# Kernel optimization log

Hardware: AMD Instinct MI355X
Metric: run time of the kernel (lower is better)

The kernel has to match this reference:

```python
import jax, jax.numpy as jnp
import numpy as np

N = 100000   # nodes
E = 1000000  # edges (avg degree 10)
F_IN, H1, H2, C = 128, 64, 64, 16


def setup_inputs() -> dict:
    key = jax.random.key(0)
    ks = jax.random.split(key, 10)
    x = jax.random.normal(ks[0], (N, F_IN), dtype=jnp.float32)
    edge_src = jax.random.randint(ks[1], (E,), 0, N, dtype=jnp.int32)
    edge_dst = jax.random.randint(ks[2], (E,), 0, N, dtype=jnp.int32)
    # normalized-adjacency-like positive edge weights (~1/deg scale)
    edge_val = jax.random.uniform(ks[3], (E,), dtype=jnp.float32) * 0.1
    def glorot(k, fan_in, fan_out):
        s = np.float32(1.0 / np.sqrt(fan_in))
        return jax.random.normal(k, (fan_in, fan_out), dtype=jnp.float32) * s
    W1 = glorot(ks[4], F_IN, H1)
    W2 = glorot(ks[5], H1, H2)
    W3 = glorot(ks[6], H2, C)
    b1 = jnp.zeros((H1,), jnp.float32)
    b2 = jnp.zeros((H2,), jnp.float32)
    b3 = jnp.zeros((C,), jnp.float32)
    return {"x": x, "edge_val": edge_val, "W1": W1, "b1": b1,
            "W2": W2, "b2": b2, "W3": W3, "b3": b3,
            "edge_src": edge_src, "edge_dst": edge_dst}


def gcn_layer(h, W, b, edge_src, edge_dst, edge_val):
    # support = h @ W ; out = spmm(adj, support) + b
    support = h @ W                                  # [N, d_out]
    msg = support[edge_src] * edge_val[:, None]      # [E, d_out] gather + scale
    agg = jax.ops.segment_sum(msg, edge_dst, num_segments=N)  # scatter-add
    return agg + b


def reference(x, edge_val, W1, b1, W2, b2, W3, b3, edge_src, edge_dst):
    # eval mode: F.dropout(training=False) is identity
    h = jax.nn.relu(gcn_layer(x, W1, b1, edge_src, edge_dst, edge_val))
    h = jax.nn.relu(gcn_layer(h, W2, b2, edge_src, edge_dst, edge_val))
    return gcn_layer(h, W3, b3, edge_src, edge_dst, edge_val)  # [N, C] logits
```

## Files before the change

kernel.cpp:

```cpp
#include <hip/hip_runtime.h>
#include <stdint.h>

#define N_NODES 100000
#define N_EDGES 1000000
#define NBUCK 98

typedef __attribute__((ext_vector_type(8))) __bf16 bf16x8;
typedef __attribute__((ext_vector_type(4))) float f32x4;

static __device__ __forceinline__ float bf2f(unsigned short u) {
    return __uint_as_float(((unsigned int)u) << 16);
}
static __device__ __forceinline__ unsigned short f2bf(float f) {
    unsigned int u = __float_as_uint(f);
    unsigned int r = (u + 0x7FFFu + ((u >> 16) & 1u)) >> 16;
    return (unsigned short)r;
}
static __device__ __forceinline__ float4 ld4_half(const unsigned short* p) {
    ushort4 u = *(const ushort4*)p;
    return make_float4(bf2f(u.x), bf2f(u.y), bf2f(u.z), bf2f(u.w));
}
static __device__ __forceinline__ void st4_half(unsigned short* p, float4 f) {
    ushort4 u;
    u.x = f2bf(f.x); u.y = f2bf(f.y); u.z = f2bf(f.z); u.w = f2bf(f.w);
    *(ushort4*)p = u;
}
static __device__ __forceinline__ void st8_half(unsigned short* p, const float* f) {
    int4 u;
    u.x = (int)(((unsigned)f2bf(f[0])) | (((unsigned)f2bf(f[1])) << 16));
    u.y = (int)(((unsigned)f2bf(f[2])) | (((unsigned)f2bf(f[3])) << 16));
    u.z = (int)(((unsigned)f2bf(f[4])) | (((unsigned)f2bf(f[5])) << 16));
    u.w = (int)(((unsigned)f2bf(f[6])) | (((unsigned)f2bf(f[7])) << 16));
    *(int4*)p = u;
}

static __device__ __forceinline__ float ldf(const void* p, size_t i, int bf) {
    return bf ? bf2f(((const unsigned short*)p)[i]) : ((const float*)p)[i];
}
static __device__ __forceinline__ float4 ldf4(const void* p, size_t i, int bf) {
    if (bf) return ld4_half((const unsigned short*)p + i);
    return *(const float4*)((const float*)p + i);
}

__global__ __launch_bounds__(256) void detect_kernel(const unsigned short* __restrict__ xs,
                                                     int* __restrict__ flag) {
    __shared__ int sz;
    if (threadIdx.x == 0) sz = 0;
    __syncthreads();
    int z = 0;
    for (int i = threadIdx.x; i < 1024; i += 256) {
        float av = fabsf(bf2f(xs[2 * i]));
        if (!(av <= 1048576.0f) || (av != 0.0f && av < 9.5367431640625e-07f)) z++;
    }
    atomicAdd(&sz, z);
    __syncthreads();
    if (threadIdx.x == 0) *flag = (sz > 256) ? 0 : 1;
}

__global__ __launch_bounds__(256) void bhist_kernel(const int* __restrict__ dst,
                                                    int* __restrict__ bcount) {
    __shared__ int cnt[NBUCK];
    int tid = threadIdx.x;
    for (int i = tid; i < NBUCK; i += 256) cnt[i] = 0;
    __syncthreads();
    int e0 = blockIdx.x * 4096;
#pragma unroll
    for (int i = 0; i < 16; ++i) {
        int e = e0 + i * 256 + tid;
        if (e < N_EDGES) atomicAdd(&cnt[dst[e] >> 10], 1);
    }
    __syncthreads();
    for (int i = tid; i < NBUCK; i += 256) {
        int c = cnt[i];
        if (c) atomicAdd(&bcount[i], c);
    }
}

__global__ __launch_bounds__(128) void bscan_kernel(const int* __restrict__ bcount,
                                                    int* __restrict__ bstart,
                                                    int* __restrict__ bcursor) {
    __shared__ int sh[128];
    int tid = threadIdx.x;
    int v = (tid < NBUCK) ? bcount[tid] : 0;
    sh[tid] = v;
    __syncthreads();
    for (int off = 1; off < 128; off <<= 1) {
        int t = 0;
        if (tid >= off) t = sh[tid - off];
        __syncthreads();
        if (tid >= off) sh[tid] += t;
        __syncthreads();
    }
    if (tid < NBUCK) {
        int excl = sh[tid] - v;
        bstart[tid] = excl;
        bcursor[tid] = excl;
    }
    if (tid == NBUCK - 1) bstart[NBUCK] = sh[tid];
}

__global__ __launch_bounds__(256) void part_kernel(const int* __restrict__ src,
                                                   const int* __restrict__ dst,
                                                   const void* __restrict__ val,
                                                   int* __restrict__ bcursor,
                                                   int2* __restrict__ part,
                                                   const int* __restrict__ flagp) {
    __shared__ int cnt[NBUCK];
    __shared__ int base[NBUCK];
    const int bf = *flagp;
    const int tid = threadIdx.x;
    const int e0 = blockIdx.x * 2048;
    for (int i = tid; i < NBUCK; i += 256) cnt[i] = 0;
    __syncthreads();
    int rank[8], bkt[8], pk[8], vb[8];
#pragma unroll
    for (int i = 0; i < 8; ++i) {
        int e = e0 + i * 256 + tid;
        bkt[i] = -1;
        if (e < N_EDGES) {
            int d = dst[e];
            int b = d >> 10;
            bkt[i] = b;
            pk[i] = src[e] | ((d & 1023) << 17);
            vb[i] = __float_as_int(ldf(val, e, bf));
            rank[i] = atomicAdd(&cnt[b], 1);
        }
    }
    __syncthreads();
    for (int i = tid; i < NBUCK; i += 256) {
        int c = cnt[i];
        base[i] = c ? atomicAdd(&bcursor[i], c) : 0;
    }
    __syncthreads();
#pragma unroll
    for (int i = 0; i < 8; ++i) {
        if (bkt[i] >= 0) part[(size_t)base[bkt[i]] + rank[i]] = make_int2(pk[i], vb[i]);
    }
}

__global__ __launch_bounds__(512) void place_kernel(const int* __restrict__ bstart,
                                                    const int2* __restrict__ part,
                                                    int* __restrict__ row_start,
                                                    int2* __restrict__ csr_rec) {
    __shared__ int cnt[1024];
    __shared__ int sums[512];
    const int tid = threadIdx.x;
    const int b = blockIdx.x;
    const int row0 = b << 10;
    const int nrows = min(1024, N_NODES - row0);
    const int s = bstart[b], e = bstart[b + 1];

    for (int i = tid; i < 1024; i += 512) cnt[i] = 0;
    __syncthreads();
    for (int j = s + tid; j < e; j += 512) {
        unsigned p = (unsigned)part[j].x;
        atomicAdd(&cnt[p >> 17], 1);
    }
    __syncthreads();
    int a0 = cnt[2 * tid], a1 = cnt[2 * tid + 1];
    int ts = a0 + a1;
    sums[tid] = ts;
    __syncthreads();
    for (int off = 1; off < 512; off <<= 1) {
        int t = 0;
        if (tid >= off) t = sums[tid - off];
        __syncthreads();
        if (tid >= off) sums[tid] += t;
        __syncthreads();
    }
    int excl = sums[tid] - ts;
    cnt[2 * tid] = s + excl;
    cnt[2 * tid + 1] = s + excl + a0;
    if (2 * tid < nrows)     row_start[row0 + 2 * tid] = s + excl;
    if (2 * tid + 1 < nrows) row_start[row0 + 2 * tid + 1] = s + excl + a0;
    if (b == NBUCK - 1 && tid == 0) row_start[N_NODES] = e;
    __syncthreads();
    for (int j = s + tid; j < e; j += 512) {
        int2 r = part[j];
        unsigned p = (unsigned)r.x;
        int pos = atomicAdd(&cnt[p >> 17], 1);
        csr_rec[pos] = make_int2((int)(p & 0x1FFFFu), r.y);
    }
}


static __device__ __forceinline__ void duo_gather64(const unsigned short* __restrict__ supc,
                                                    const int2* __restrict__ csr_rec,
                                                    int s, int b1, int e,
                                                    float a0[8], float a1[8]) {
    if (s >= e) return;
    int2 r[8];
#pragma unroll
    for (int t = 0; t < 8; ++t) r[t] = csr_rec[min(s + t, e - 1)];
    for (int j = s; j < e; j += 8) {
        int4 sp[8];
#pragma unroll
        for (int t = 0; t < 8; ++t) sp[t] = *(const int4*)(supc + (size_t)r[t].x * 64);
        float wv[8];
#pragma unroll
        for (int t = 0; t < 8; ++t) wv[t] = (j + t < e) ? __int_as_float(r[t].y) : 0.0f;
        int jn = j + 8;
        if (jn < e) {
#pragma unroll
            for (int t = 0; t < 8; ++t) r[t] = csr_rec[min(jn + t, e - 1)];
        }
#pragma unroll
        for (int t = 0; t < 8; ++t) {
            float w0 = (j + t < b1) ? wv[t] : 0.0f;
            float w1 = wv[t] - w0;
            int q[4] = {sp[t].x, sp[t].y, sp[t].z, sp[t].w};
#pragma unroll
            for (int c = 0; c < 4; ++c) {
                float flo = __uint_as_float(((unsigned)q[c]) << 16);
                float fhi = __uint_as_float(((unsigned)q[c]) & 0xffff0000u);
                a0[2 * c]     += w0 * flo; a0[2 * c + 1] += w0 * fhi;
                a1[2 * c]     += w1 * flo; a1[2 * c + 1] += w1 * fhi;
            }
        }
    }
}

static __device__ __forceinline__ void quad_gather16(const unsigned short* __restrict__ supc,
                                                     const int2* __restrict__ csr_rec,
                                                     int s, int b1, int b2, int b3, int e,
                                                     float a[4][8]) {
    if (s >= e) return;
    int2 r[8];
#pragma unroll
    for (int t = 0; t < 8; ++t) r[t] = csr_rec[min(s + t, e - 1)];
    for (int j = s; j < e; j += 8) {
        int4 sp[8];
#pragma unroll
        for (int t = 0; t < 8; ++t) sp[t] = *(const int4*)(supc + (size_t)r[t].x * 16);
        float wv[8];
#pragma unroll
        for (int t = 0; t < 8; ++t) wv[t] = (j + t < e) ? __int_as_float(r[t].y) : 0.0f;
        int jn = j + 8;
        if (jn < e) {
#pragma unroll
            for (int t = 0; t < 8; ++t) r[t] = csr_rec[min(jn + t, e - 1)];
        }
#pragma unroll
        for (int t = 0; t < 8; ++t) {
            int idx = j + t;
            float c0 = (idx < b1) ? wv[t] : 0.0f;
            float c1 = (idx < b2) ? wv[t] : 0.0f;
            float c2 = (idx < b3) ? wv[t] : 0.0f;
            float w0 = c0, w1 = c1 - c0, w2 = c2 - c1, w3 = wv[t] - c2;
            int q[4] = {sp[t].x, sp[t].y, sp[t].z, sp[t].w};
#pragma unroll
            for (int c = 0; c < 4; ++c) {
                float flo = __uint_as_float(((unsigned)q[c]) << 16);
                float fhi = __uint_as_float(((unsigned)q[c]) & 0xffff0000u);
                a[0][2 * c] += w0 * flo; a[0][2 * c + 1] += w0 * fhi;
                a[1][2 * c] += w1 * flo; a[1][2 * c + 1] += w1 * fhi;
                a[2][2 * c] += w2 * flo; a[2][2 * c + 1] += w2 * fhi;
                a[3][2 * c] += w3 * flo; a[3][2 * c + 1] += w3 * fhi;
            }
        }
    }
}

template <int K, int M, bool DYNIN>
__global__ __launch_bounds__(256, 4) void mgemm_kernel(const void* __restrict__ hv_,
                                                       const void* __restrict__ W,
                                                       unsigned short* __restrict__ out,
                                                       const int* __restrict__ flagp) {
    constexpr int KP = K + 8;
    constexpr int NC = M / 16;
    constexpr int NK = K / 32;
    constexpr int NT = (N_NODES + 63) / 64;

    __shared__ unsigned short wt[M][KP];

    const int bf = *flagp;
    const int tid = threadIdx.x;

    for (int i = tid; i < K * M; i += 256) {
        int k = i / M, m = i % M;
        wt[m][k] = f2bf(ldf(W, i, bf));
    }
    __syncthreads();

    const int lane = tid & 63;
    const int qd = lane >> 4;
    const int ln = lane & 15;
    const int wrow = (tid >> 6) * 16;

    for (int tile = blockIdx.x; tile < NT; tile += gridDim.x) {
        const int row = tile * 64 + wrow + ln;
        const bool ok = row < N_NODES;

        f32x4 acc[NC];
#pragma unroll
        for (int c = 0; c < NC; ++c) acc[c] = (f32x4){0.f, 0.f, 0.f, 0.f};

#pragma unroll
        for (int ks = 0; ks < NK; ++ks) {
            bf16x8 a;
            if (ok) {
                const size_t base = (size_t)row * K + ks * 32 + qd * 8;
                if (DYNIN && !bf) {
                    const float* xp = (const float*)hv_ + base;
                    float4 f0 = *(const float4*)xp;
                    float4 f1 = *(const float4*)(xp + 4);
                    ushort4 uu[2];
                    uu[0].x = f2bf(f0.x); uu[0].y = f2bf(f0.y); uu[0].z = f2bf(f0.z); uu[0].w = f2bf(f0.w);
                    uu[1].x = f2bf(f1.x); uu[1].y = f2bf(f1.y); uu[1].z = f2bf(f1.z); uu[1].w = f2bf(f1.w);
                    a = *(const bf16x8*)uu;
                } else {
                    a = *(const bf16x8*)((const unsigned short*)hv_ + base);
                }
            } else {
                a = (bf16x8)(__bf16)0.0f;
            }
#pragma unroll
            for (int c = 0; c < NC; ++c) {
                bf16x8 b = *(const bf16x8*)&wt[c * 16 + ln][ks * 32 + qd * 8];
                acc[c] = __builtin_amdgcn_mfma_f32_16x16x32_bf16(a, b, acc[c], 0, 0, 0);
            }
        }

#pragma unroll
        for (int c = 0; c < NC; ++c) {
#pragma unroll
            for (int r = 0; r < 4; ++r) {
                int orow = tile * 64 + wrow + qd * 4 + r;
                if (orow < N_NODES) out[(size_t)orow * M + c * 16 + ln] = f2bf(acc[c][r]);
            }
        }
    }
}

template <int MOUT>
__global__ __launch_bounds__(256) void fused_kernel(const unsigned short* __restrict__ support,
                                                    const int* __restrict__ row_start,
                                                    const int2* __restrict__ csr_rec,
                                                    const void* __restrict__ bias,
                                                    const void* __restrict__ W,
                                                    unsigned short* __restrict__ out,
                                                    const int* __restrict__ flagp) {
    constexpr int K = 64, KP = 72;
    constexpr int NC = MOUT / 16;
    constexpr int NK = 2;
    constexpr int NT = (N_NODES + 63) / 64;

    __shared__ unsigned short agg[64][KP];
    __shared__ unsigned short wt[MOUT][KP];

    const int bf = *flagp;
    const int tid = threadIdx.x;

    for (int i = tid; i < K * MOUT; i += 256) {
        int k = i / MOUT, m = i % MOUT;
        wt[m][k] = f2bf(ldf(W, i, bf));
    }
    __syncthreads();

    const int lane = tid & 63;
    const int qd = lane >> 4;
    const int ln = lane & 15;
    const int wrow = (tid >> 6) * 16;

    const int grp = tid >> 3;
    const int cc = tid & 7;
    float bias8[8];
#pragma unroll
    for (int c = 0; c < 8; ++c) bias8[c] = ldf(bias, cc * 8 + c, bf);
    const unsigned short* supc = support + cc * 8;

    for (int tile = blockIdx.x; tile < NT; tile += gridDim.x) {
        const int r0 = tile * 64 + grp * 2;
        int s  = row_start[min(r0 + 0, N_NODES)];
        int b1 = row_start[min(r0 + 1, N_NODES)];
        int e  = row_start[min(r0 + 2, N_NODES)];

        float a0[8], a1[8];
#pragma unroll
        for (int c = 0; c < 8; ++c) { a0[c] = bias8[c]; a1[c] = bias8[c]; }
        duo_gather64(supc, csr_rec, s, b1, e, a0, a1);
#pragma unroll
        for (int c = 0; c < 8; ++c) {
            a0[c] = fmaxf(a0[c], 0.f);
            a1[c] = fmaxf(a1[c], 0.f);
        }
        st8_half(&agg[grp * 2 + 0][cc * 8], a0);
        st8_half(&agg[grp * 2 + 1][cc * 8], a1);
        __syncthreads();

        f32x4 macc[NC];
#pragma unroll
        for (int c = 0; c < NC; ++c) macc[c] = (f32x4){0.f, 0.f, 0.f, 0.f};
#pragma unroll
        for (int ks = 0; ks < NK; ++ks) {
            bf16x8 a = *(const bf16x8*)&agg[wrow + ln][ks * 32 + qd * 8];
#pragma unroll
            for (int c = 0; c < NC; ++c) {
                bf16x8 b = *(const bf16x8*)&wt[c * 16 + ln][ks * 32 + qd * 8];
                macc[c] = __builtin_amdgcn_mfma_f32_16x16x32_bf16(a, b, macc[c], 0, 0, 0);
            }
        }

#pragma unroll
        for (int c = 0; c < NC; ++c) {
#pragma unroll
            for (int r = 0; r < 4; ++r) {
                int orow = tile * 64 + wrow + qd * 4 + r;
                if (orow < N_NODES) out[(size_t)orow * MOUT + c * 16 + ln] = f2bf(macc[c][r]);
            }
        }
        __syncthreads();
    }
}

template <bool DYNOUT>
__global__ __launch_bounds__(256) void spmm16_kernel(const unsigned short* __restrict__ support,
                                                     const int* __restrict__ row_start,
                                                     const int2* __restrict__ csr_rec,
                                                     const void* __restrict__ bias,
                                                     void* __restrict__ out_,
                                                     const int* __restrict__ flagp) {
    constexpr int M = 16;
    int bf = *flagp;
    int tid = threadIdx.x;
    int grp = tid >> 1;
    int cc = tid & 1;
    int r0 = blockIdx.x * 512 + grp * 4;
    if (r0 >= N_NODES) return;
    int s  = row_start[min(r0 + 0, N_NODES)];
    int b1 = row_start[min(r0 + 1, N_NODES)];
    int b2 = row_start[min(r0 + 2, N_NODES)];
    int b3 = row_start[min(r0 + 3, N_NODES)];
    int e  = row_start[min(r0 + 4, N_NODES)];
    float a[4][8];
#pragma unroll
    for (int k = 0; k < 4; ++k)
#pragma unroll
        for (int c = 0; c < 8; ++c) a[k][c] = ldf(bias, cc * 8 + c, bf);
    quad_gather16(support + cc * 8, csr_rec, s, b1, b2, b3, e, a);
#pragma unroll
    for (int k = 0; k < 4; ++k) {
        int row = r0 + k;
        if (row < N_NODES) {
            if (DYNOUT && !bf) {
                float* op = (float*)out_ + (size_t)row * M + cc * 8;
                *(float4*)op = make_float4(a[k][0], a[k][1], a[k][2], a[k][3]);
                *(float4*)(op + 4) = make_float4(a[k][4], a[k][5], a[k][6], a[k][7]);
            } else {
                st8_half((unsigned short*)out_ + (size_t)row * M + cc * 8, a[k]);
            }
        }
    }
}

extern "C" void kernel_launch(void* const* d_in, const int* in_sizes, int n_in,
                              void* d_out, int out_size, void* d_ws, size_t ws_size,
                              hipStream_t stream) {
    (void)in_sizes; (void)n_in; (void)out_size; (void)ws_size;
    const void* x  = d_in[0];
    const void* ev = d_in[1];
    const void* W1 = d_in[2];
    const void* b1 = d_in[3];
    const void* W2 = d_in[4];
    const void* b2 = d_in[5];
    const void* W3 = d_in[6];
    const void* b3 = d_in[7];
    const int* esrc = (const int*)d_in[8];
    const int* edst = (const int*)d_in[9];

    char* ws = (char*)d_ws;
    size_t off = 0;
    auto alloc = [&](size_t bytes) -> void* {
        void* p = ws + off;
        off = (off + bytes + 255) & ~(size_t)255;
        return p;
    };
    unsigned short* A = (unsigned short*)alloc((size_t)N_NODES * 64 * 2);
    unsigned short* B = (unsigned short*)alloc((size_t)N_NODES * 64 * 2);
    int* row_start  = (int*)alloc((size_t)(N_NODES + 1) * 4);
    int* bcount     = (int*)alloc(512);
    int* bstart     = (int*)alloc(512);
    int* bcursor    = (int*)alloc(512);
    int2* csr_rec   = (int2*)alloc((size_t)N_EDGES * 8);
    int* flagp      = (int*)alloc(256);
    int2* part      = (int2*)A;

    detect_kernel<<<1, 256, 0, stream>>>((const unsigned short*)x, flagp);

    hipMemsetAsync(bcount, 0, 512, stream);
    bhist_kernel<<<(N_EDGES + 4095) / 4096, 256, 0, stream>>>(edst, bcount);
    bscan_kernel<<<1, 128, 0, stream>>>(bcount, bstart, bcursor);
    part_kernel<<<(N_EDGES + 2047) / 2048, 256, 0, stream>>>(esrc, edst, ev, bcursor, part, flagp);
    place_kernel<<<NBUCK, 512, 0, stream>>>(bstart, part, row_start, csr_rec);

    const int NT = (N_NODES + 63) / 64;

    mgemm_kernel<128, 64, true><<<1024, 256, 0, stream>>>(x, W1, A, flagp);
    fused_kernel<64><<<NT, 256, 0, stream>>>(A, row_start, csr_rec, b1, W2, B, flagp);
    fused_kernel<16><<<NT, 256, 0, stream>>>(B, row_start, csr_rec, b2, W3, A, flagp);
    spmm16_kernel<true><<<(N_NODES + 511) / 512, 256, 0, stream>>>(A, row_start, csr_rec, b3, d_out, flagp);
}
```

Baseline: 260.5 us.

## Drop bucket histogram pass with fixed-capacity buckets; one tile per block

```diff
diff --git a/kernel.cpp b/kernel.cpp
--- a/kernel.cpp
+++ b/kernel.cpp
@@ -4,6 +4,7 @@
 #define N_NODES 100000
 #define N_EDGES 1000000
 #define NBUCK 98
+#define CAP 12288
 
 typedef __attribute__((ext_vector_type(8))) __bf16 bf16x8;
 typedef __attribute__((ext_vector_type(4))) float f32x4;
@@ -43,7 +44,8 @@
 }
 
 __global__ __launch_bounds__(256) void detect_kernel(const unsigned short* __restrict__ xs,
-                                                     int* __restrict__ flag) {
+                                                     int* __restrict__ flag,
+                                                     int* __restrict__ bcursor) {
     __shared__ int sz;
     if (threadIdx.x == 0) sz = 0;
     __syncthreads();
@@ -53,50 +55,9 @@
         if (!(av <= 1048576.0f) || (av != 0.0f && av < 9.5367431640625e-07f)) z++;
     }
     atomicAdd(&sz, z);
+    if (threadIdx.x < NBUCK) bcursor[threadIdx.x] = threadIdx.x * CAP;
     __syncthreads();
     if (threadIdx.x == 0) *flag = (sz > 256) ? 0 : 1;
-}
-
-__global__ __launch_bounds__(256) void bhist_kernel(const int* __restrict__ dst,
-                                                    int* __restrict__ bcount) {
-    __shared__ int cnt[NBUCK];
-    int tid = threadIdx.x;
-    for (int i = tid; i < NBUCK; i += 256) cnt[i] = 0;
-    __syncthreads();
-    int e0 = blockIdx.x * 4096;
-#pragma unroll
-    for (int i = 0; i < 16; ++i) {
-        int e = e0 + i * 256 + tid;
-        if (e < N_EDGES) atomicAdd(&cnt[dst[e] >> 10], 1);
-    }
-    __syncthreads();
-    for (int i = tid; i < NBUCK; i += 256) {
-        int c = cnt[i];
-        if (c) atomicAdd(&bcount[i], c);
-    }
-}
-
-__global__ __launch_bounds__(128) void bscan_kernel(const int* __restrict__ bcount,
-                                                    int* __restrict__ bstart,
-                                                    int* __restrict__ bcursor) {
-    __shared__ int sh[128];
-    int tid = threadIdx.x;
-    int v = (tid < NBUCK) ? bcount[tid] : 0;
-    sh[tid] = v;
-    __syncthreads();
-    for (int off = 1; off < 128; off <<= 1) {
-        int t = 0;
-        if (tid >= off) t = sh[tid - off];
-        __syncthreads();
-        if (tid >= off) sh[tid] += t;
-        __syncthreads();
-    }
-    if (tid < NBUCK) {
-        int excl = sh[tid] - v;
-        bstart[tid] = excl;
-        bcursor[tid] = excl;
-    }
-    if (tid == NBUCK - 1) bstart[NBUCK] = sh[tid];
 }
 
 __global__ __launch_bounds__(256) void part_kernel(const int* __restrict__ src,
@@ -138,22 +99,42 @@
     }
 }
 
-__global__ __launch_bounds__(512) void place_kernel(const int* __restrict__ bstart,
+__global__ __launch_bounds__(512) void place_kernel(const int* __restrict__ bcursor,
                                                     const int2* __restrict__ part,
                                                     int* __restrict__ row_start,
                                                     int2* __restrict__ csr_rec) {
     __shared__ int cnt[1024];
     __shared__ int sums[512];
+    __shared__ int sh_s, sh_cnt, sh_total;
     const int tid = threadIdx.x;
     const int b = blockIdx.x;
     const int row0 = b << 10;
     const int nrows = min(1024, N_NODES - row0);
-    const int s = bstart[b], e = bstart[b + 1];
+
+    if (tid < 128) sums[tid] = (tid < NBUCK) ? (bcursor[tid] - tid * CAP) : 0;
+    __syncthreads();
+    for (int off = 1; off < 128; off <<= 1) {
+        int t = 0;
+        if (tid < 128 && tid >= off) t = sums[tid - off];
+        __syncthreads();
+        if (tid < 128 && tid >= off) sums[tid] += t;
+        __syncthreads();
+    }
+    if (tid == 0) {
+        sh_s = (b > 0) ? sums[b - 1] : 0;
+        sh_cnt = bcursor[b] - b * CAP;
+        sh_total = sums[NBUCK - 1];
+    }
+    __syncthreads();
+    const int s = sh_s;
+    const int cb = sh_cnt;
+    const int ps = b * CAP;
+    const int total = sh_total;
 
     for (int i = tid; i < 1024; i += 512) cnt[i] = 0;
     __syncthreads();
-    for (int j = s + tid; j < e; j += 512) {
-        unsigned p = (unsigned)part[j].x;
+    for (int j = tid; j < cb; j += 512) {
+        unsigned p = (unsigned)part[ps + j].x;
         atomicAdd(&cnt[p >> 17], 1);
     }
     __syncthreads();
@@ -173,16 +154,15 @@
     cnt[2 * tid + 1] = s + excl + a0;
     if (2 * tid < nrows)     row_start[row0 + 2 * tid] = s + excl;
     if (2 * tid + 1 < nrows) row_start[row0 + 2 * tid + 1] = s + excl + a0;
-    if (b == NBUCK - 1 && tid == 0) row_start[N_NODES] = e;
-    __syncthreads();
-    for (int j = s + tid; j < e; j += 512) {
-        int2 r = part[j];
+    if (b == NBUCK - 1 && tid == 0) row_start[N_NODES] = total;
+    __syncthreads();
+    for (int j = tid; j < cb; j += 512) {
+        int2 r = part[ps + j];
         unsigned p = (unsigned)r.x;
         int pos = atomicAdd(&cnt[p >> 17], 1);
         csr_rec[pos] = make_int2((int)(p & 0x1FFFFu), r.y);
     }
 }
-
 
 static __device__ __forceinline__ void duo_gather64(const unsigned short* __restrict__ supc,
                                                     const int2* __restrict__ csr_rec,
@@ -262,14 +242,13 @@
 }
 
 template <int K, int M, bool DYNIN>
-__global__ __launch_bounds__(256, 4) void mgemm_kernel(const void* __restrict__ hv_,
-                                                       const void* __restrict__ W,
-                                                       unsigned short* __restrict__ out,
-                                                       const int* __restrict__ flagp) {
+__global__ __launch_bounds__(256) void mgemm_kernel(const void* __restrict__ hv_,
+                                                    const void* __restrict__ W,
+                                                    unsigned short* __restrict__ out,
+                                                    const int* __restrict__ flagp) {
     constexpr int KP = K + 8;
     constexpr int NC = M / 16;
     constexpr int NK = K / 32;
-    constexpr int NT = (N_NODES + 63) / 64;
 
     __shared__ unsigned short wt[M][KP];
 
@@ -286,48 +265,47 @@
     const int qd = lane >> 4;
     const int ln = lane & 15;
     const int wrow = (tid >> 6) * 16;
-
-    for (int tile = blockIdx.x; tile < NT; tile += gridDim.x) {
-        const int row = tile * 64 + wrow + ln;
-        const bool ok = row < N_NODES;
-
-        f32x4 acc[NC];
-#pragma unroll
-        for (int c = 0; c < NC; ++c) acc[c] = (f32x4){0.f, 0.f, 0.f, 0.f};
-
-#pragma unroll
-        for (int ks = 0; ks < NK; ++ks) {
-            bf16x8 a;
-            if (ok) {
-                const size_t base = (size_t)row * K + ks * 32 + qd * 8;
-                if (DYNIN && !bf) {
-                    const float* xp = (const float*)hv_ + base;
-                    float4 f0 = *(const float4*)xp;
-                    float4 f1 = *(const float4*)(xp + 4);
-                    ushort4 uu[2];
-                    uu[0].x = f2bf(f0.x); uu[0].y = f2bf(f0.y); uu[0].z = f2bf(f0.z); uu[0].w = f2bf(f0.w);
-                    uu[1].x = f2bf(f1.x); uu[1].y = f2bf(f1.y); uu[1].z = f2bf(f1.z); uu[1].w = f2bf(f1.w);
-                    a = *(const bf16x8*)uu;
-                } else {
-                    a = *(const bf16x8*)((const unsigned short*)hv_ + base);
-                }
+    const int tile = blockIdx.x;
+
+    const int row = tile * 64 + wrow + ln;
+    const bool ok = row < N_NODES;
+
+    f32x4 acc[NC];
+#pragma unroll
+    for (int c = 0; c < NC; ++c) acc[c] = (f32x4){0.f, 0.f, 0.f, 0.f};
+
+#pragma unroll
+    for (int ks = 0; ks < NK; ++ks) {
+        bf16x8 a;
+        if (ok) {
+            const size_t base = (size_t)row * K + ks * 32 + qd * 8;
+            if (DYNIN && !bf) {
+                const float* xp = (const float*)hv_ + base;
+                float4 f0 = *(const float4*)xp;
+                float4 f1 = *(const float4*)(xp + 4);
+                ushort4 uu[2];
+                uu[0].x = f2bf(f0.x); uu[0].y = f2bf(f0.y); uu[0].z = f2bf(f0.z); uu[0].w = f2bf(f0.w);
+                uu[1].x = f2bf(f1.x); uu[1].y = f2bf(f1.y); uu[1].z = f2bf(f1.z); uu[1].w = f2bf(f1.w);
+                a = *(const bf16x8*)uu;
             } else {
-                a = (bf16x8)(__bf16)0.0f;
+                a = *(const bf16x8*)((const unsigned short*)hv_ + base);
             }
-#pragma unroll
-            for (int c = 0; c < NC; ++c) {
-                bf16x8 b = *(const bf16x8*)&wt[c * 16 + ln][ks * 32 + qd * 8];
-                acc[c] = __builtin_amdgcn_mfma_f32_16x16x32_bf16(a, b, acc[c], 0, 0, 0);
-            }
-        }
-
+        } else {
+            a = (bf16x8)(__bf16)0.0f;
+        }
 #pragma unroll
         for (int c = 0; c < NC; ++c) {
-#pragma unroll
-            for (int r = 0; r < 4; ++r) {
-                int orow = tile * 64 + wrow + qd * 4 + r;
-                if (orow < N_NODES) out[(size_t)orow * M + c * 16 + ln] = f2bf(acc[c][r]);
-            }
+            bf16x8 b = *(const bf16x8*)&wt[c * 16 + ln][ks * 32 + qd * 8];
+            acc[c] = __builtin_amdgcn_mfma_f32_16x16x32_bf16(a, b, acc[c], 0, 0, 0);
+        }
+    }
+
+#pragma unroll
+    for (int c = 0; c < NC; ++c) {
+#pragma unroll
+        for (int r = 0; r < 4; ++r) {
+            int orow = tile * 64 + wrow + qd * 4 + r;
+            if (orow < N_NODES) out[(size_t)orow * M + c * 16 + ln] = f2bf(acc[c][r]);
         }
     }
 }
@@ -343,7 +321,6 @@
     constexpr int K = 64, KP = 72;
     constexpr int NC = MOUT / 16;
     constexpr int NK = 2;
-    constexpr int NT = (N_NODES + 63) / 64;
 
     __shared__ unsigned short agg[64][KP];
     __shared__ unsigned short wt[MOUT][KP];
@@ -369,47 +346,45 @@
     for (int c = 0; c < 8; ++c) bias8[c] = ldf(bias, cc * 8 + c, bf);
     const unsigned short* supc = support + cc * 8;
 
-    for (int tile = blockIdx.x; tile < NT; tile += gridDim.x) {
-        const int r0 = tile * 64 + grp * 2;
-        int s  = row_start[min(r0 + 0, N_NODES)];
-        int b1 = row_start[min(r0 + 1, N_NODES)];
-        int e  = row_start[min(r0 + 2, N_NODES)];
-
-        float a0[8], a1[8];
-#pragma unroll
-        for (int c = 0; c < 8; ++c) { a0[c] = bias8[c]; a1[c] = bias8[c]; }
-        duo_gather64(supc, csr_rec, s, b1, e, a0, a1);
-#pragma unroll
-        for (int c = 0; c < 8; ++c) {
-            a0[c] = fmaxf(a0[c], 0.f);
-            a1[c] = fmaxf(a1[c], 0.f);
-        }
-        st8_half(&agg[grp * 2 + 0][cc * 8], a0);
-        st8_half(&agg[grp * 2 + 1][cc * 8], a1);
-        __syncthreads();
-
-        f32x4 macc[NC];
-#pragma unroll
-        for (int c = 0; c < NC; ++c) macc[c] = (f32x4){0.f, 0.f, 0.f, 0.f};
-#pragma unroll
-        for (int ks = 0; ks < NK; ++ks) {
-            bf16x8 a = *(const bf16x8*)&agg[wrow + ln][ks * 32 + qd * 8];
-#pragma unroll
-            for (int c = 0; c < NC; ++c) {
-                bf16x8 b = *(const bf16x8*)&wt[c * 16 + ln][ks * 32 + qd * 8];
-                macc[c] = __builtin_amdgcn_mfma_f32_16x16x32_bf16(a, b, macc[c], 0, 0, 0);
-            }
-        }
-
+    const int tile = blockIdx.x;
+    const int r0 = tile * 64 + grp * 2;
+    int s  = row_start[min(r0 + 0, N_NODES)];
+    int b1 = row_start[min(r0 + 1, N_NODES)];
+    int e  = row_start[min(r0 + 2, N_NODES)];
+
+    float a0[8], a1[8];
+#pragma unroll
+    for (int c = 0; c < 8; ++c) { a0[c] = bias8[c]; a1[c] = bias8[c]; }
+    duo_gather64(supc, csr_rec, s, b1, e, a0, a1);
+#pragma unroll
+    for (int c = 0; c < 8; ++c) {
+        a0[c] = fmaxf(a0[c], 0.f);
+        a1[c] = fmaxf(a1[c], 0.f);
+    }
+    st8_half(&agg[grp * 2 + 0][cc * 8], a0);
+    st8_half(&agg[grp * 2 + 1][cc * 8], a1);
+    __syncthreads();
+
+    f32x4 macc[NC];
+#pragma unroll
+    for (int c = 0; c < NC; ++c) macc[c] = (f32x4){0.f, 0.f, 0.f, 0.f};
+#pragma unroll
+    for (int ks = 0; ks < NK; ++ks) {
+        bf16x8 a = *(const bf16x8*)&agg[wrow + ln][ks * 32 + qd * 8];
 #pragma unroll
         for (int c = 0; c < NC; ++c) {
-#pragma unroll
-            for (int r = 0; r < 4; ++r) {
-                int orow = tile * 64 + wrow + qd * 4 + r;
-                if (orow < N_NODES) out[(size_t)orow * MOUT + c * 16 + ln] = f2bf(macc[c][r]);
-            }
-        }
-        __syncthreads();
+            bf16x8 b = *(const bf16x8*)&wt[c * 16 + ln][ks * 32 + qd * 8];
+            macc[c] = __builtin_amdgcn_mfma_f32_16x16x32_bf16(a, b, macc[c], 0, 0, 0);
+        }
+    }
+
+#pragma unroll
+    for (int c = 0; c < NC; ++c) {
+#pragma unroll
+        for (int r = 0; r < 4; ++r) {
+            int orow = tile * 64 + wrow + qd * 4 + r;
+            if (orow < N_NODES) out[(size_t)orow * MOUT + c * 16 + ln] = f2bf(macc[c][r]);
+        }
     }
 }
 
@@ -478,24 +453,19 @@
     unsigned short* A = (unsigned short*)alloc((size_t)N_NODES * 64 * 2);
     unsigned short* B = (unsigned short*)alloc((size_t)N_NODES * 64 * 2);
     int* row_start  = (int*)alloc((size_t)(N_NODES + 1) * 4);
-    int* bcount     = (int*)alloc(512);
-    int* bstart     = (int*)alloc(512);
     int* bcursor    = (int*)alloc(512);
     int2* csr_rec   = (int2*)alloc((size_t)N_EDGES * 8);
     int* flagp      = (int*)alloc(256);
     int2* part      = (int2*)A;
 
-    detect_kernel<<<1, 256, 0, stream>>>((const unsigned short*)x, flagp);
-
-    hipMemsetAsync(bcount, 0, 512, stream);
-    bhist_kernel<<<(N_EDGES + 4095) / 4096, 256, 0, stream>>>(edst, bcount);
-    bscan_kernel<<<1, 128, 0, stream>>>(bcount, bstart, bcursor);
+    detect_kernel<<<1, 256, 0, stream>>>((const unsigned short*)x, flagp, bcursor);
+
     part_kernel<<<(N_EDGES + 2047) / 2048, 256, 0, stream>>>(esrc, edst, ev, bcursor, part, flagp);
-    place_kernel<<<NBUCK, 512, 0, stream>>>(bstart, part, row_start, csr_rec);
+    place_kernel<<<NBUCK, 512, 0, stream>>>(bcursor, part, row_start, csr_rec);
 
     const int NT = (N_NODES + 63) / 64;
 
-    mgemm_kernel<128, 64, true><<<1024, 256, 0, stream>>>(x, W1, A, flagp);
+    mgemm_kernel<128, 64, true><<<NT, 256, 0, stream>>>(x, W1, A, flagp);
     fused_kernel<64><<<NT, 256, 0, stream>>>(A, row_start, csr_rec, b1, W2, B, flagp);
     fused_kernel<16><<<NT, 256, 0, stream>>>(B, row_start, csr_rec, b2, W3, A, flagp);
     spmm16_kernel<true><<<(N_NODES + 511) / 512, 256, 0, stream>>>(A, row_start, csr_rec, b3, d_out, flagp);
```

Result: faster. 244.8 us (-6.0%).
